# Performance work log

Measured on AMD Instinct MI355X. Metric: run time of the kernel, lower is better.

## Reference

```python
import jax, jax.numpy as jnp
import numpy as np

K = 16  # kNN neighbors (KnnEncoder default)


def _bn(h, g, s):
    # eval-mode BatchNorm with running mean 0 / var 1 folded into affine
    return h * g + s


def setup_inputs() -> dict:
    key = jax.random.key(0)
    cnt = [0]
    def nk():
        cnt[0] += 1
        return jax.random.fold_in(key, cnt[0])
    B, N = 4, 4096
    def W(i, o):
        return jax.random.normal(nk(), (i, o), jnp.float32) / np.float32(i) ** 0.5
    def bias(d):
        return jnp.zeros((d,), jnp.float32)
    def gamma(d):
        return jnp.ones((d,), jnp.float32) + 0.1 * jax.random.normal(nk(), (d,), jnp.float32)
    def beta(d):
        return 0.1 * jax.random.normal(nk(), (d,), jnp.float32)
    inp = dict(
        pos=jax.random.normal(nk(), (B, N, 3), jnp.float32),
        query_point_idx=jax.random.randint(nk(), (B,), 0, N),
        # PointNetConv local MLP: 6 -> 64 -> 128 -> 256 (plain last)
        cw1=W(6, 64), cb1=bias(64), cg1=gamma(64), cs1=beta(64),
        cw2=W(64, 128), cb2=bias(128), cg2=gamma(128), cs2=beta(128),
        cw3=W(128, 256), cb3=bias(256),
        # GlobalSAModule MLP: 259 -> 256 -> 512 -> 1024 (plain last)
        sw1=W(259, 256), sb1=bias(256), sg1=gamma(256), ss1=beta(256),
        sw2=W(256, 512), sb2=bias(512), sg2=gamma(512), ss2=beta(512),
        sw3=W(512, 1024), sb3=bias(1024),
        # EdgeGraspPredictor: 1280 -> 512 -> 256 -> 16
        pw1=W(1280, 512), pb1=bias(512),
        pw2=W(512, 256), pb2=bias(256),
        pw3=W(256, 16), pb3=bias(16),
    )
    return inp


def reference(pos, query_point_idx, cw1, cb1, cg1, cs1, cw2, cb2, cg2, cs2, cw3, cb3,
              sw1, sb1, sg1, ss1, sw2, sb2, sg2, ss2, sw3, sb3,
              pw1, pb1, pw2, pb2, pw3, pb3):
    B, N, _ = pos.shape
    # kNN within each cloud (self included, as torch_geometric knn with x==y)
    d2 = jnp.sum((pos[:, :, None, :] - pos[:, None, :, :]) ** 2, axis=-1)  # [B,N,N]
    _, idx = jax.lax.top_k(-d2, K)  # [B,N,K] targets for each source point n
    nbr = jax.vmap(lambda p, i: p[i])(pos, idx)  # [B,N,K,3] target positions
    # PointNetConv message: cat([x_j = pos_src, pos_src - pos_tgt])
    src = jnp.broadcast_to(pos[:, :, None, :], (B, N, K, 3))
    h = jnp.concatenate([src, src - nbr], axis=-1)  # [B,N,K,6]
    h = jnp.maximum(_bn(h @ cw1 + cb1, cg1, cs1), 0.0)
    h = jnp.maximum(_bn(h @ cw2 + cb2, cg2, cs2), 0.0)
    m = h @ cw3 + cb3  # [B,N,K,256] per-edge messages
    # scatter-max aggregation at target nodes (every node has its self edge)
    tgt = (idx + (jnp.arange(B) * N)[:, None, None]).reshape(-1)
    x = jax.ops.segment_max(m.reshape(-1, m.shape[-1]), tgt, num_segments=B * N)
    x = x.reshape(B, N, -1)  # [B,N,256] per-point features
    # GlobalSAModule: pointwise MLP then global max pool per cloud
    g = jnp.concatenate([x, pos], axis=-1)  # [B,N,259]
    g = jnp.maximum(_bn(g @ sw1 + sb1, sg1, ss1), 0.0)
    g = jnp.maximum(_bn(g @ sw2 + sb2, sg2, ss2), 0.0)
    g = g @ sw3 + sb3  # [B,N,1024]
    scene = jnp.max(g, axis=1)  # [B,1024]
    # gather query point feature, concat with scene feature, predictor MLP
    q = query_point_idx + jnp.arange(B) * N
    point_feat = x.reshape(B * N, -1)[q]  # [B,256]
    ef = jnp.concatenate([point_feat, scene], axis=-1)  # [B,1280]
    h = jnp.maximum(ef @ pw1 + pb1, 0.0)
    h = jnp.maximum(h @ pw2 + pb2, 0.0)
    return h @ pw3 + pb3  # [B,16]
```

## Files before the change

kernel.cpp:

```cpp
#include <hip/hip_runtime.h>

#define BB 4
#define NN 4096
#define KK 16

typedef unsigned short u16;
typedef unsigned int   u32;
typedef unsigned long long u64;

typedef __attribute__((ext_vector_type(8))) short bf16x8;
typedef __attribute__((ext_vector_type(4))) float f32x4;

__device__ __forceinline__ float b2f(u16 x){ return __uint_as_float(((u32)x) << 16); }
__device__ __forceinline__ u16 f2b(float f){
    u32 u = __float_as_uint(f);
    u32 r = (u + 0x7FFFu + ((u >> 16) & 1u)) >> 16;
    return (u16)r;
}
__device__ __forceinline__ u32 fmap(float f){
    u32 u = __float_as_uint(f);
    return (u & 0x80000000u) ? ~u : (u | 0x80000000u);
}
__device__ __forceinline__ float funmap(u32 u){
    u32 v = (u & 0x80000000u) ? (u ^ 0x80000000u) : ~u;
    return __uint_as_float(v);
}

#define N_ARR 27
__device__ const int ASZ[N_ARR] = {
    49152, 384, 64, 64, 64, 8192, 128, 128, 128, 32768, 256,
    66304, 256, 256, 256, 131072, 512, 512, 512, 524288, 1024,
    655360, 512, 131072, 256, 4096, 16 };
__device__ const int AOFF[N_ARR] = {
    0, 49152, 49536, 49600, 49664, 49728, 57920, 58048, 58176, 58304, 91072,
    91328, 157632, 157888, 158144, 158400, 289472, 289984, 290496, 291008, 815296,
    816320, 1471680, 1472192, 1603264, 1603520, 1607616 };

struct Ptrs { const void* p[N_ARR]; };

#define O_POS 0
#define O_CW1 49152
#define O_CB1 49536
#define O_CG1 49600
#define O_CS1 49664
#define O_CB2 57920
#define O_CG2 58048
#define O_CS2 58176
#define O_CB3 91072
#define O_SW1 91328
#define O_SB1 157632
#define O_SG1 157888
#define O_SS1 158144
#define O_SB2 289472
#define O_SG2 289984
#define O_SS2 290496
#define O_SB3 815296
#define O_PW1 816320
#define O_PB1 1471680
#define O_PW2 1472192
#define O_PB2 1603264
#define O_PW3 1603520
#define O_PB3 1607616

__global__ void detect_kernel(const u16* __restrict__ pos_u16, u32* __restrict__ flag){
    __shared__ int cnt;
    if (threadIdx.x == 0) cnt = 0;
    __syncthreads();
    int c = 0;
    #pragma unroll
    for (int s = 0; s < 4; ++s){
        u16 u = pos_u16[2*(threadIdx.x*4 + s)];
        int e = (u >> 7) & 0xFF;
        c += (e >= 0x68 && e <= 0x82) ? 1 : 0;
    }
    atomicAdd(&cnt, c);
    __syncthreads();
    if (threadIdx.x == 0) *flag = (cnt >= 512) ? 1u : 0u;
}

__device__ __forceinline__ void pack_one_src(const void* __restrict__ src, bool isbf,
                                             u16* __restrict__ dst, int tot, int log2n,
                                             int g, int T){
    const int nmask = (1 << log2n) - 1;
    for (int id = g; id < tot; id += T){
        int i = id & 7, lg = (id >> 3) & 3;
        int rest = id >> 5;
        int n = rest & nmask;
        int ks = rest >> log2n;
        int si = (ks*32 + lg*8 + i) << log2n | n;
        dst[id] = isbf ? ((const u16*)src)[si] : f2b(((const float*)src)[si]);
    }
}

__global__ __launch_bounds__(256) void prep_kernel(Ptrs pt, const u32* __restrict__ flagp,
        float* __restrict__ dst, float* __restrict__ psoa,
        u16* __restrict__ wp2, u16* __restrict__ wp3,
        u16* __restrict__ swp1, u16* __restrict__ swp2, u16* __restrict__ swp3){
    const bool isbf = (*flagp != 0);
    const int T = gridDim.x * 256;
    const int g = blockIdx.x * 256 + threadIdx.x;
    #pragma unroll
    for (int a = 0; a < N_ARR; ++a){
        if (a == 5 || a == 9 || a == 15 || a == 19) continue;
        const int sz = ASZ[a], off = AOFF[a];
        if (isbf){
            const u16* s = (const u16*)pt.p[a];
            for (int i = g; i < sz; i += T) dst[off + i] = b2f(s[i]);
        } else {
            const float* s = (const float*)pt.p[a];
            for (int i = g; i < sz; i += T) dst[off + i] = s[i];
        }
    }
    for (int i = g; i < BB*NN; i += T){
        float x, y, z;
        if (isbf){
            const u16* s = (const u16*)pt.p[0];
            x = b2f(s[3*i]); y = b2f(s[3*i+1]); z = b2f(s[3*i+2]);
        } else {
            const float* s = (const float*)pt.p[0];
            x = s[3*i]; y = s[3*i+1]; z = s[3*i+2];
        }
        psoa[i] = x; psoa[BB*NN + i] = y; psoa[2*BB*NN + i] = z;
    }
    pack_one_src(pt.p[5],  isbf, wp2,    8192,  7, g, T);
    pack_one_src(pt.p[9],  isbf, wp3,   32768,  8, g, T);
    pack_one_src(pt.p[11], isbf, swp1,  65536,  8, g, T);
    pack_one_src(pt.p[15], isbf, swp2, 131072,  9, g, T);
    pack_one_src(pt.p[19], isbf, swp3, 524288, 10, g, T);
}

#define QCAP 192
__device__ __forceinline__ void refine16(u64* __restrict__ buf, int& cnt, float& tau, int lane){
    u64 loc[3];
    #pragma unroll
    for (int q = 0; q < 3; ++q){
        int p = lane + (q << 6);
        loc[q] = (p < cnt) ? buf[p] : ~0ull;
    }
    u64 m = ~0ull;
    #pragma unroll
    for (int r = 0; r < KK; ++r){
        m = loc[0];
        m = loc[1] < m ? loc[1] : m;
        m = loc[2] < m ? loc[2] : m;
        #pragma unroll
        for (int off = 32; off > 0; off >>= 1){
            u64 o = __shfl_xor(m, off);
            m = o < m ? o : m;
        }
        if (lane == r) buf[r] = m;
        #pragma unroll
        for (int q = 0; q < 3; ++q) if (loc[q] == m) loc[q] = ~0ull;
    }
    cnt = KK;
    tau = __uint_as_float((u32)(m >> 32));
}

__global__ __launch_bounds__(512) void knn_kernel(const float* __restrict__ psoa,
                                                  int* __restrict__ knn_out,
                                                  u32* __restrict__ deg){
    __shared__ __align__(16) u64 kbuf[16*QCAP];
    const int b  = blockIdx.x >> 8;
    const int i0 = (blockIdx.x & 255) << 4;
    const float* px = psoa + b*NN;
    const float* py = psoa + BB*NN + b*NN;
    const float* pz = psoa + 2*BB*NN + b*NN;
    const int tid = threadIdx.x;
    const int lane = tid & 63;
    const int wv = tid >> 6;
    const int iA = i0 + wv*2, iB = iA + 1;
    const float ax = px[iA], ay = py[iA], az = pz[iA];
    const float bx = px[iB], by = py[iB], bz = pz[iB];
    u64* bufA = kbuf + (wv*2)*QCAP;
    u64* bufB = bufA + QCAP;

    float tauA = 3.0e38f, tauB = 3.0e38f;
    int cntA = 0, cntB = 0;
    for (int t = 0; t < 64; t += 8){
        float cx[8], cy[8], cz[8];
        #pragma unroll
        for (int c = 0; c < 8; ++c){
            int j = lane + ((t + c) << 6);
            cx[c] = px[j]; cy[c] = py[j]; cz[c] = pz[j];
        }
        #pragma unroll
        for (int c = 0; c < 8; ++c){
            int j = lane + ((t + c) << 6);
            float dxA = ax - cx[c], dyA = ay - cy[c], dzA = az - cz[c];
            float d2A = __fadd_rn(__fadd_rn(__fmul_rn(dxA,dxA), __fmul_rn(dyA,dyA)), __fmul_rn(dzA,dzA));
            float dxB = bx - cx[c], dyB = by - cy[c], dzB = bz - cz[c];
            float d2B = __fadd_rn(__fadd_rn(__fmul_rn(dxB,dxB), __fmul_rn(dyB,dyB)), __fmul_rn(dzB,dzB));
            bool pA = (d2A <= tauA);
            u64 balA = __ballot(pA);
            if (balA){
                int nins = __popcll(balA);
                if (cntA + nins > QCAP) refine16(bufA, cntA, tauA, lane);
                if (pA){
                    int ofs = __popcll(balA & ((1ull << lane) - 1ull));
                    bufA[cntA + ofs] = (((u64)__float_as_uint(d2A)) << 32) | (u32)j;
                }
                cntA += nins;
            }
            bool pB = (d2B <= tauB);
            u64 balB = __ballot(pB);
            if (balB){
                int nins = __popcll(balB);
                if (cntB + nins > QCAP) refine16(bufB, cntB, tauB, lane);
                if (pB){
                    int ofs = __popcll(balB & ((1ull << lane) - 1ull));
                    bufB[cntB + ofs] = (((u64)__float_as_uint(d2B)) << 32) | (u32)j;
                }
                cntB += nins;
            }
        }
    }
    refine16(bufA, cntA, tauA, lane);
    refine16(bufB, cntB, tauB, lane);
    if (lane < KK){
        u64 kA = bufA[lane];
        int jA = (int)(u32)(kA & 0xFFFFFFFFu);
        knn_out[((size_t)(b*NN + iA))*KK + lane] = jA;
        atomicAdd(deg + (b << 12) + jA, 1u);
        u64 kB = bufB[lane];
        int jB = (int)(u32)(kB & 0xFFFFFFFFu);
        knn_out[((size_t)(b*NN + iB))*KK + lane] = jB;
        atomicAdd(deg + (b << 12) + jB, 1u);
    }
}

__global__ __launch_bounds__(1024) void scan_kernel(const u32* __restrict__ deg,
                                                    int* __restrict__ rowstart, u32* __restrict__ cursor){
    __shared__ int lsum[1024];
    const int tid = threadIdx.x;
    const int base = tid * 16;
    int loc[16]; int s = 0;
    #pragma unroll
    for (int q = 0; q < 16; ++q){ loc[q] = (int)deg[base+q]; s += loc[q]; }
    lsum[tid] = s;
    __syncthreads();
    int acc = s;
    for (int ofs = 1; ofs < 1024; ofs <<= 1){
        int t = (tid >= ofs) ? lsum[tid-ofs] : 0;
        __syncthreads();
        acc += t; lsum[tid] = acc;
        __syncthreads();
    }
    int excl = acc - s;
    #pragma unroll
    for (int q = 0; q < 16; ++q){
        rowstart[base+q] = excl; cursor[base+q] = (u32)excl; excl += loc[q];
    }
    if (tid == 1023) rowstart[16384] = excl;
}

__global__ __launch_bounds__(256) void fill_kernel(const int* __restrict__ knn,
                                                   u32* __restrict__ cursor, int* __restrict__ csr){
    int e = blockIdx.x*256 + threadIdx.x;
    int b = e >> 16;
    int t = (b << 12) + knn[e];
    u32 pos = atomicAdd(cursor + t, 1u);
    csr[pos] = e;
}

__device__ __forceinline__ bf16x8 ldfrag(const u16* h, int row, int kofs, int rowstride){
    u32 byte = (u32)((row*rowstride + kofs)*2) ^ (u32)((row & 7) << 4);
    return *(const bf16x8*)((const char*)h + byte);
}
__device__ __forceinline__ void st16(u16* h, int row, int col, int rowstride, float v){
    u32 byte = (u32)((row*rowstride + col)*2) ^ (u32)((row & 7) << 4);
    *(u16*)((char*)h + byte) = f2b(v);
}

__global__ __launch_bounds__(256, 2) void edge_kernel(
    const float* __restrict__ conv, const int* __restrict__ knn,
    const int* __restrict__ rowstart, const int* __restrict__ csr,
    const u16* __restrict__ wp2, const u16* __restrict__ wp3,
    u16* __restrict__ xh)
{
    __shared__ float in6[6][64];
    __shared__ int   lts[64];
    __shared__ int   rs_l[17];
    __shared__ float scw1[384];
    __shared__ float sc1[64], sh1[64];
    __shared__ __align__(16) u16 h1s[64*64];
    __shared__ __align__(16) u16 h2s[64*128];
    __shared__ u32 lsx[16*256];

    const float* posf = conv + O_POS;
    const float* cb1 = conv + O_CB1; const float* cg1 = conv + O_CG1; const float* cs1 = conv + O_CS1;

    const int tid = threadIdx.x;
    const int w   = tid >> 6;
    const int l   = tid & 63;
    const int t0  = blockIdx.x << 4;
    const int b   = t0 >> 12;

    if (tid < 64){ float g1 = cg1[tid]; sc1[tid]=g1; sh1[tid]=cb1[tid]*g1 + cs1[tid]; }
    if (tid < 17) rs_l[tid] = rowstart[t0 + tid];
    for (int u = tid; u < 384; u += 256) scw1[u] = conv[O_CW1 + u];
    #pragma unroll
    for (int q = 0; q < 16; ++q) lsx[q*256 + tid] = 0u;

    const int lr = l & 15, lg = l >> 4;
    const int colb2 = w << 5;
    const int colb3 = w << 6;

    float sc2v[2], sh2v[2], bs3v[4];
    #pragma unroll
    for (int nt = 0; nt < 2; ++nt){
        int c = colb2 + nt*16 + lr;
        float g2 = conv[O_CG2 + c];
        sc2v[nt] = g2; sh2v[nt] = conv[O_CB2 + c]*g2 + conv[O_CS2 + c];
    }
    #pragma unroll
    for (int nt = 0; nt < 4; ++nt) bs3v[nt] = conv[O_CB3 + colb3 + nt*16 + lr];

    __syncthreads();
    const int segstart = rs_l[0], segend = rs_l[16];
    const int nchunk = (segend - segstart + 63) >> 6;

    int curl = -1;
    float run[4];
    #pragma unroll
    for (int nt = 0; nt < 4; ++nt) run[nt] = 0.f;

    for (int ch = 0; ch < nchunk; ++ch){
        __syncthreads();
        if (tid < 64){
            int gpos = segstart + (ch << 6) + tid;
            int lt = -1;
            float ax=0,ay=0,az=0,dx=0,dy=0,dz=0;
            if (gpos < segend){
                lt = 0;
                #pragma unroll
                for (int q = 1; q < 16; ++q) lt += (gpos >= rs_l[q]) ? 1 : 0;
                int e = csr[gpos];
                int i = (e >> 4) & (NN - 1);
                int j = knn[e];
                const float* pi = posf + ((size_t)(b*NN + i))*3;
                const float* pj = posf + ((size_t)(b*NN + j))*3;
                ax = pi[0]; ay = pi[1]; az = pi[2];
                dx = ax - pj[0]; dy = ay - pj[1]; dz = az - pj[2];
            }
            lts[tid] = lt;
            in6[0][tid]=ax; in6[1][tid]=ay; in6[2][tid]=az;
            in6[3][tid]=dx; in6[4][tid]=dy; in6[5][tid]=dz;
        }
        __syncthreads();

        {
            const int e = tid & 63, c0g = (tid >> 6) << 4;
            float a0=in6[0][e], a1=in6[1][e], a2=in6[2][e],
                  a3=in6[3][e], a4=in6[4][e], a5=in6[5][e];
            u32 pk[8];
            #pragma unroll
            for (int ci = 0; ci < 16; ++ci){
                int cc = c0g + ci;
                float acc = a0*scw1[cc]     + a1*scw1[64+cc]  + a2*scw1[128+cc]
                          + a3*scw1[192+cc] + a4*scw1[256+cc] + a5*scw1[320+cc];
                float v = fmaxf(acc*sc1[cc] + sh1[cc], 0.f);
                u32 h = (u32)f2b(v);
                if (ci & 1) pk[ci >> 1] |= h << 16; else pk[ci >> 1] = h;
            }
            u32 base = (u32)(e*128 + c0g*2);
            u32 swz  = (u32)((e & 7) << 4);
            *(uint4*)((char*)h1s + (base ^ swz))        = make_uint4(pk[0],pk[1],pk[2],pk[3]);
            *(uint4*)((char*)h1s + ((base + 16) ^ swz)) = make_uint4(pk[4],pk[5],pk[6],pk[7]);
        }
        __syncthreads();

        {
            f32x4 acc2[4][2];
            #pragma unroll
            for (int mt = 0; mt < 4; ++mt)
                #pragma unroll
                for (int nt = 0; nt < 2; ++nt) acc2[mt][nt] = (f32x4){0.f,0.f,0.f,0.f};
            #pragma unroll
            for (int ks = 0; ks < 2; ++ks){
                bf16x8 bf[2];
                #pragma unroll
                for (int nt = 0; nt < 2; ++nt)
                    bf[nt] = *(const bf16x8*)(wp2 + (((ks*128 + colb2 + nt*16 + lr) << 2) + lg)*8);
                #pragma unroll
                for (int mt = 0; mt < 4; ++mt){
                    bf16x8 a = ldfrag(h1s, mt*16 + lr, ks*32 + lg*8, 64);
                    #pragma unroll
                    for (int nt = 0; nt < 2; ++nt)
                        acc2[mt][nt] = __builtin_amdgcn_mfma_f32_16x16x32_bf16(a, bf[nt], acc2[mt][nt], 0, 0, 0);
                }
            }
            #pragma unroll
            for (int mt = 0; mt < 4; ++mt)
                #pragma unroll
                for (int nt = 0; nt < 2; ++nt)
                    #pragma unroll
                    for (int r = 0; r < 4; ++r){
                        int row = mt*16 + lg*4 + r;
                        float v = fmaxf(acc2[mt][nt][r]*sc2v[nt] + sh2v[nt], 0.f);
                        st16(h2s, row, colb2 + nt*16 + lr, 128, v);
                    }
        }
        __syncthreads();

        {
            f32x4 acc3[4][4];
            #pragma unroll
            for (int mt = 0; mt < 4; ++mt)
                #pragma unroll
                for (int nt = 0; nt < 4; ++nt) acc3[mt][nt] = (f32x4){0.f,0.f,0.f,0.f};
            #pragma unroll
            for (int ks = 0; ks < 4; ++ks){
                bf16x8 bf[4];
                #pragma unroll
                for (int nt = 0; nt < 4; ++nt)
                    bf[nt] = *(const bf16x8*)(wp3 + (((ks*256 + colb3 + nt*16 + lr) << 2) + lg)*8);
                #pragma unroll
                for (int mt = 0; mt < 4; ++mt){
                    bf16x8 a = ldfrag(h2s, mt*16 + lr, ks*32 + lg*8, 128);
                    #pragma unroll
                    for (int nt = 0; nt < 4; ++nt)
                        acc3[mt][nt] = __builtin_amdgcn_mfma_f32_16x16x32_bf16(a, bf[nt], acc3[mt][nt], 0, 0, 0);
                }
            }
            #pragma unroll
            for (int mt = 0; mt < 4; ++mt)
                #pragma unroll
                for (int r = 0; r < 4; ++r){
                    int row = mt*16 + lg*4 + r;
                    int lt = lts[row];
                    if (lt != curl){
                        if (curl >= 0){
                            #pragma unroll
                            for (int nt = 0; nt < 4; ++nt)
                                atomicMax(&lsx[curl*256 + colb3 + nt*16 + lr], fmap(run[nt]));
                        }
                        curl = lt;
                        #pragma unroll
                        for (int nt = 0; nt < 4; ++nt) run[nt] = acc3[mt][nt][r] + bs3v[nt];
                    } else {
                        #pragma unroll
                        for (int nt = 0; nt < 4; ++nt) run[nt] = fmaxf(run[nt], acc3[mt][nt][r] + bs3v[nt]);
                    }
                }
        }
    }
    if (curl >= 0){
        #pragma unroll
        for (int nt = 0; nt < 4; ++nt)
            atomicMax(&lsx[curl*256 + colb3 + nt*16 + lr], fmap(run[nt]));
    }
    __syncthreads();
    #pragma unroll
    for (int q = 0; q < 16; ++q)
        xh[((size_t)(t0+q))*256 + tid] = f2b(funmap(lsx[q*256 + tid]));
}

__global__ __launch_bounds__(256, 3) void sa_kernel(
    const float* __restrict__ conv, const u16* __restrict__ xh,
    const u16* __restrict__ swp1, const u16* __restrict__ swp2, const u16* __restrict__ swp3,
    u32* __restrict__ scene_map)
{
    __shared__ __align__(16) u16 h1s[32*256];
    __shared__ __align__(16) u16 h2s[32*512];
    __shared__ float spw[3][256];
    __shared__ float spx[32], spy[32], spz[32];

    const int tid = threadIdx.x;
    const int w   = tid >> 6;
    const int l   = tid & 63;
    const int lr  = l & 15, lg = l >> 4;
    const int b   = blockIdx.x >> 7;
    const int n0  = (blockIdx.x & 127) << 5;
    const u16* xrow = xh + ((size_t)(b*NN + n0))*256;

    if (tid < 96){
        int p = tid & 31, d = tid >> 5;
        float v = conv[O_POS + ((size_t)(b*NN + n0 + p))*3 + d];
        if (d == 0) spx[p] = v; else if (d == 1) spy[p] = v; else spz[p] = v;
    }
    for (int u = tid; u < 768; u += 256)
        spw[u >> 8][u & 255] = conv[O_SW1 + (256 + (u >> 8))*256 + (u & 255)];
    __syncthreads();

    {
        const int c0 = w << 6;
        float sc1v[4], sh1v[4];
        #pragma unroll
        for (int nt = 0; nt < 4; ++nt){
            int cc = c0 + nt*16 + lr;
            float g = conv[O_SG1 + cc];
            sc1v[nt] = g; sh1v[nt] = conv[O_SB1 + cc]*g + conv[O_SS1 + cc];
        }
        f32x4 acc[2][4];
        #pragma unroll
        for (int mt = 0; mt < 2; ++mt)
            #pragma unroll
            for (int nt = 0; nt < 4; ++nt)
                #pragma unroll
                for (int r = 0; r < 4; ++r){
                    int row = mt*16 + lg*4 + r;
                    int cc  = c0 + nt*16 + lr;
                    acc[mt][nt][r] = spx[row]*spw[0][cc] + spy[row]*spw[1][cc] + spz[row]*spw[2][cc];
                }
        #pragma unroll
        for (int ks = 0; ks < 8; ++ks){
            bf16x8 bf[4];
            #pragma unroll
            for (int nt = 0; nt < 4; ++nt)
                bf[nt] = *(const bf16x8*)(swp1 + (((ks*256 + c0 + nt*16 + lr) << 2) + lg)*8);
            #pragma unroll
            for (int mt = 0; mt < 2; ++mt){
                bf16x8 a = *(const bf16x8*)(xrow + (mt*16 + lr)*256 + ks*32 + lg*8);
                #pragma unroll
                for (int nt = 0; nt < 4; ++nt)
                    acc[mt][nt] = __builtin_amdgcn_mfma_f32_16x16x32_bf16(a, bf[nt], acc[mt][nt], 0, 0, 0);
            }
        }
        #pragma unroll
        for (int mt = 0; mt < 2; ++mt)
            #pragma unroll
            for (int nt = 0; nt < 4; ++nt)
                #pragma unroll
                for (int r = 0; r < 4; ++r){
                    int row = mt*16 + lg*4 + r;
                    float v = fmaxf(acc[mt][nt][r]*sc1v[nt] + sh1v[nt], 0.f);
                    st16(h1s, row, c0 + nt*16 + lr, 256, v);
                }
    }
    __syncthreads();

    {
        const int c0 = w << 7;
        float sc2v[8], sh2v[8];
        #pragma unroll
        for (int nt = 0; nt < 8; ++nt){
            int cc = c0 + nt*16 + lr;
            float g = conv[O_SG2 + cc];
            sc2v[nt] = g; sh2v[nt] = conv[O_SB2 + cc]*g + conv[O_SS2 + cc];
        }
        f32x4 acc[2][8];
        #pragma unroll
        for (int mt = 0; mt < 2; ++mt)
            #pragma unroll
            for (int nt = 0; nt < 8; ++nt) acc[mt][nt] = (f32x4){0.f,0.f,0.f,0.f};
        #pragma unroll
        for (int ks = 0; ks < 8; ++ks){
            bf16x8 bf[8];
            #pragma unroll
            for (int nt = 0; nt < 8; ++nt)
                bf[nt] = *(const bf16x8*)(swp2 + (((ks*512 + c0 + nt*16 + lr) << 2) + lg)*8);
            #pragma unroll
            for (int mt = 0; mt < 2; ++mt){
                bf16x8 a = ldfrag(h1s, mt*16 + lr, ks*32 + lg*8, 256);
                #pragma unroll
                for (int nt = 0; nt < 8; ++nt)
                    acc[mt][nt] = __builtin_amdgcn_mfma_f32_16x16x32_bf16(a, bf[nt], acc[mt][nt], 0, 0, 0);
            }
        }
        #pragma unroll
        for (int mt = 0; mt < 2; ++mt)
            #pragma unroll
            for (int nt = 0; nt < 8; ++nt)
                #pragma unroll
                for (int r = 0; r < 4; ++r){
                    int row = mt*16 + lg*4 + r;
                    float v = fmaxf(acc[mt][nt][r]*sc2v[nt] + sh2v[nt], 0.f);
                    st16(h2s, row, c0 + nt*16 + lr, 512, v);
                }
    }
    __syncthreads();

    #pragma unroll
    for (int half = 0; half < 2; ++half){
        const int c0 = (half << 9) + (w << 7);
        f32x4 acc[2][8];
        #pragma unroll
        for (int mt = 0; mt < 2; ++mt)
            #pragma unroll
            for (int nt = 0; nt < 8; ++nt) acc[mt][nt] = (f32x4){0.f,0.f,0.f,0.f};
        #pragma unroll
        for (int ks = 0; ks < 16; ++ks){
            bf16x8 bf[8];
            #pragma unroll
            for (int nt = 0; nt < 8; ++nt)
                bf[nt] = *(const bf16x8*)(swp3 + (((ks*1024 + c0 + nt*16 + lr) << 2) + lg)*8);
            #pragma unroll
            for (int mt = 0; mt < 2; ++mt){
                bf16x8 a = ldfrag(h2s, mt*16 + lr, ks*32 + lg*8, 512);
                #pragma unroll
                for (int nt = 0; nt < 8; ++nt)
                    acc[mt][nt] = __builtin_amdgcn_mfma_f32_16x16x32_bf16(a, bf[nt], acc[mt][nt], 0, 0, 0);
            }
        }
        #pragma unroll
        for (int nt = 0; nt < 8; ++nt){
            float v = acc[0][nt][0];
            #pragma unroll
            for (int mt = 0; mt < 2; ++mt)
                #pragma unroll
                for (int r = 0; r < 4; ++r) v = fmaxf(v, acc[mt][nt][r]);
            v = fmaxf(v, __shfl_xor(v, 16));
            v = fmaxf(v, __shfl_xor(v, 32));
            if (lg == 0){
                int cc = c0 + nt*16 + lr;
                atomicMax(scene_map + (b << 10) + cc, fmap(v + conv[O_SB3 + cc]));
            }
        }
    }
}

__global__ __launch_bounds__(128) void head1_kernel(
    const float* __restrict__ conv,
    const u16* __restrict__ xh, const u32* __restrict__ scene_map, const int* __restrict__ qidx,
    float* __restrict__ h1out)
{
    __shared__ float ef[1280];
    __shared__ float psum[4][32];
    const float* pw1 = conv + O_PW1; const float* pb1 = conv + O_PB1;
    const int b  = blockIdx.x >> 4;
    const int c0 = (blockIdx.x & 15) << 5;
    const int tid = threadIdx.x;
    const int q = qidx[b];
    for (int u = tid; u < 1280; u += 128){
        float v;
        if (u < 256) v = b2f(xh[(((size_t)(b*NN + q)) << 8) + u]);
        else         v = funmap(scene_map[(b << 10) + (u - 256)]);
        ef[u] = v;
    }
    __syncthreads();
    const int c = c0 + (tid & 31);
    const int rc = tid >> 5;
    float acc = 0.f;
    for (int r = rc*320; r < rc*320 + 320; ++r) acc += ef[r] * pw1[r*512 + c];
    psum[rc][tid & 31] = acc;
    __syncthreads();
    if (tid < 32){
        float a = psum[0][tid] + psum[1][tid] + psum[2][tid] + psum[3][tid] + pb1[c0 + tid];
        h1out[(b << 9) + c0 + tid] = fmaxf(a, 0.f);
    }
}

__global__ __launch_bounds__(256) void head2_kernel(
    const float* __restrict__ conv, const float* __restrict__ h1in,
    const u32* __restrict__ flagp, void* __restrict__ outv)
{
    __shared__ float h1[4][512];
    __shared__ float h2[4][256];
    const float* pw2 = conv + O_PW2; const float* pb2 = conv + O_PB2;
    const float* pw3 = conv + O_PW3; const float* pb3 = conv + O_PB3;
    const int tid = threadIdx.x;
    for (int u = tid; u < 2048; u += 256) h1[u >> 9][u & 511] = h1in[u];
    __syncthreads();
    for (int o = tid; o < 1024; o += 256){
        int b = o >> 8, c = o & 255;
        float acc = pb2[c];
        for (int r = 0; r < 512; ++r) acc += h1[b][r] * pw2[r*256 + c];
        h2[b][c] = fmaxf(acc, 0.f);
    }
    __syncthreads();
    if (tid < 64){
        int b = tid >> 4, c = tid & 15;
        float acc = pb3[c];
        for (int r = 0; r < 256; ++r) acc += h2[b][r] * pw3[r*16 + c];
        if (*flagp) ((u16*)outv)[tid] = f2b(acc);
        else        ((float*)outv)[tid] = acc;
    }
}

extern "C" void kernel_launch(void* const* d_in, const int* in_sizes, int n_in,
                              void* d_out, int out_size, void* d_ws, size_t ws_size,
                              hipStream_t stream){
    (void)in_sizes; (void)n_in; (void)out_size; (void)ws_size;
    const int* qidx = (const int*)d_in[1];

    char* ws = (char*)d_ws;
    u32*  flag      = (u32*)ws;
    float* conv     = (float*)(ws + 1024);
    u16*  wp2       = (u16*)(ws + 6432768);
    u16*  wp3       = (u16*)(ws + 6449152);
    u16*  swp1      = (u16*)(ws + 6514688);
    u16*  swp2      = (u16*)(ws + 6645760);
    u16*  swp3      = (u16*)(ws + 6907904);
    int*  knn       = (int*)(ws + 7956480);
    u32*  deg       = (u32*)(ws + 9005056);
    u32*  scene_map = (u32*)(ws + 9070592);
    int*  rowstart  = (int*)(ws + 9086976);
    u32*  cursor    = (u32*)(ws + 9152576);
    int*  csr       = (int*)(ws + 9218112);
    u16*  xh        = (u16*)(ws + 10266688);
    float* h1ws     = (float*)(ws + 18655296);
    float* psoa     = (float*)(ws + 18663488);

    Ptrs pt;
    pt.p[0] = d_in[0];
    for (int k = 1; k < N_ARR; ++k) pt.p[k] = d_in[k + 1];

    hipMemsetAsync(ws + 9005056, 0, 81920, stream);

    detect_kernel <<<1, 256, 0, stream>>>((const u16*)d_in[0], flag);
    prep_kernel   <<<512, 256, 0, stream>>>(pt, flag, conv, psoa, wp2, wp3, swp1, swp2, swp3);
    knn_kernel <<<1024, 512, 0, stream>>>(psoa, knn, deg);
    scan_kernel<<<1, 1024, 0, stream>>>(deg, rowstart, cursor);
    fill_kernel<<<1024, 256, 0, stream>>>(knn, cursor, csr);
    edge_kernel<<<1024, 256, 0, stream>>>(conv, knn, rowstart, csr, wp2, wp3, xh);
    sa_kernel  <<<512, 256, 0, stream>>>(conv, xh, swp1, swp2, swp3, scene_map);
    head1_kernel<<<64, 128, 0, stream>>>(conv, xh, scene_map, qidx, h1ws);
    head2_kernel<<<1, 256, 0, stream>>>(conv, h1ws, flag, (void*)d_out);
}
```

Baseline: 371.0 us.

## Sort points by x and prune kNN search with a sweep-window bound

Adds a per-cloud bitonic sort of points by x coordinate, then has the kNN kernel scan candidates outward from each query's sorted position. The scan stops once the x-gap on both sides exceeds the current 16th-nearest distance. This replaces the brute-force scan of all 4096 candidates per query with a pruned scan. It adds a sort kernel running on only 4 blocks, and the pruning can be weak for 3D Gaussian data sorted on one axis. Tie ordering among equal distances may differ because indices are remapped through the sort.

```diff
diff --git a/kernel.cpp b/kernel.cpp
--- a/kernel.cpp
+++ b/kernel.cpp
@@ -129,6 +129,40 @@
     pack_one_src(pt.p[19], isbf, swp3, 524288, 10, g, T);
 }
 
+__global__ __launch_bounds__(1024) void sort_kernel(const float* __restrict__ psoa,
+        float* __restrict__ xs, float* __restrict__ ys, float* __restrict__ zs,
+        int* __restrict__ sidx){
+    __shared__ u64 s[NN];
+    const int b = blockIdx.x;
+    const int tid = threadIdx.x;
+    const float* px = psoa + b*NN;
+    const float* py = psoa + BB*NN + b*NN;
+    const float* pz = psoa + 2*BB*NN + b*NN;
+    for (int i = tid; i < NN; i += 1024)
+        s[i] = (((u64)fmap(px[i])) << 32) | (u32)i;
+    __syncthreads();
+    for (int ksz = 2; ksz <= NN; ksz <<= 1){
+        for (int jj = ksz >> 1; jj > 0; jj >>= 1){
+            for (int t = tid; t < NN/2; t += 1024){
+                int i  = ((t & ~(jj-1)) << 1) | (t & (jj-1));
+                int ix = i | jj;
+                u64 a = s[i], v = s[ix];
+                bool up = ((i & ksz) == 0);
+                if ((a > v) == up){ s[i] = v; s[ix] = a; }
+            }
+            __syncthreads();
+        }
+    }
+    for (int r = tid; r < NN; r += 1024){
+        u64 kv = s[r];
+        int oi = (int)(u32)(kv & 0xFFFFFFFFu);
+        xs[b*NN + r] = funmap((u32)(kv >> 32));
+        ys[b*NN + r] = py[oi];
+        zs[b*NN + r] = pz[oi];
+        sidx[b*NN + r] = oi;
+    }
+}
+
 #define QCAP 192
 __device__ __forceinline__ void refine16(u64* __restrict__ buf, int& cnt, float& tau, int lane){
     u64 loc[3];
@@ -156,74 +190,80 @@
     tau = __uint_as_float((u32)(m >> 32));
 }
 
-__global__ __launch_bounds__(512) void knn_kernel(const float* __restrict__ psoa,
-                                                  int* __restrict__ knn_out,
-                                                  u32* __restrict__ deg){
+__global__ __launch_bounds__(512) void knn_kernel(
+        const float* __restrict__ xs, const float* __restrict__ ys,
+        const float* __restrict__ zs, const int* __restrict__ sidx,
+        int* __restrict__ knn_out, u32* __restrict__ deg){
     __shared__ __align__(16) u64 kbuf[16*QCAP];
     const int b  = blockIdx.x >> 8;
-    const int i0 = (blockIdx.x & 255) << 4;
-    const float* px = psoa + b*NN;
-    const float* py = psoa + BB*NN + b*NN;
-    const float* pz = psoa + 2*BB*NN + b*NN;
+    const int r0 = (blockIdx.x & 255) << 4;
+    const float* X = xs + b*NN;
+    const float* Y = ys + b*NN;
+    const float* Z = zs + b*NN;
+    const int*   S = sidx + b*NN;
     const int tid = threadIdx.x;
     const int lane = tid & 63;
     const int wv = tid >> 6;
-    const int iA = i0 + wv*2, iB = iA + 1;
-    const float ax = px[iA], ay = py[iA], az = pz[iA];
-    const float bx = px[iB], by = py[iB], bz = pz[iB];
+    const int rA = r0 + wv*2, rB = rA + 1;
+    const float axq = X[rA], ayq = Y[rA], azq = Z[rA];
+    const float bxq = X[rB], byq = Y[rB], bzq = Z[rB];
     u64* bufA = kbuf + (wv*2)*QCAP;
     u64* bufB = bufA + QCAP;
 
     float tauA = 3.0e38f, tauB = 3.0e38f;
     int cntA = 0, cntB = 0;
-    for (int t = 0; t < 64; t += 8){
-        float cx[8], cy[8], cz[8];
-        #pragma unroll
-        for (int c = 0; c < 8; ++c){
-            int j = lane + ((t + c) << 6);
-            cx[c] = px[j]; cy[c] = py[j]; cz[c] = pz[j];
-        }
-        #pragma unroll
-        for (int c = 0; c < 8; ++c){
-            int j = lane + ((t + c) << 6);
-            float dxA = ax - cx[c], dyA = ay - cy[c], dzA = az - cz[c];
-            float d2A = __fadd_rn(__fadd_rn(__fmul_rn(dxA,dxA), __fmul_rn(dyA,dyA)), __fmul_rn(dzA,dzA));
-            float dxB = bx - cx[c], dyB = by - cy[c], dzB = bz - cz[c];
-            float d2B = __fadd_rn(__fadd_rn(__fmul_rn(dxB,dxB), __fmul_rn(dyB,dyB)), __fmul_rn(dzB,dzB));
-            bool pA = (d2A <= tauA);
-            u64 balA = __ballot(pA);
-            if (balA){
-                int nins = __popcll(balA);
-                if (cntA + nins > QCAP) refine16(bufA, cntA, tauA, lane);
-                if (pA){
-                    int ofs = __popcll(balA & ((1ull << lane) - 1ull));
-                    bufA[cntA + ofs] = (((u64)__float_as_uint(d2A)) << 32) | (u32)j;
-                }
-                cntA += nins;
-            }
-            bool pB = (d2B <= tauB);
-            u64 balB = __ballot(pB);
-            if (balB){
-                int nins = __popcll(balB);
-                if (cntB + nins > QCAP) refine16(bufB, cntB, tauB, lane);
-                if (pB){
-                    int ofs = __popcll(balB & ((1ull << lane) - 1ull));
-                    bufB[cntB + ofs] = (((u64)__float_as_uint(d2B)) << 32) | (u32)j;
-                }
-                cntB += nins;
-            }
-        }
+    for (int k = 0; k < 128; ++k){
+        int j = (lane < 32) ? (rA - 1 - (k << 5) - lane)
+                            : (rA + (k << 5) + (lane - 32));
+        bool inr = ((u32)j < (u32)NN);
+        int ja = inr ? j : rA;
+        float cx = X[ja], cy = Y[ja], cz = Z[ja];
+        int sorig = S[ja];
+        float dxA = axq - cx, dyA = ayq - cy, dzA = azq - cz;
+        float d2A = __fadd_rn(__fadd_rn(__fmul_rn(dxA,dxA), __fmul_rn(dyA,dyA)), __fmul_rn(dzA,dzA));
+        float dxB = bxq - cx, dyB = byq - cy, dzB = bzq - cz;
+        float d2B = __fadd_rn(__fadd_rn(__fmul_rn(dxB,dxB), __fmul_rn(dyB,dyB)), __fmul_rn(dzB,dzB));
+        bool pA = inr && (d2A <= tauA);
+        u64 balA = __ballot(pA);
+        if (balA){
+            int nins = __popcll(balA);
+            if (cntA + nins > QCAP) refine16(bufA, cntA, tauA, lane);
+            if (pA){
+                int ofs = __popcll(balA & ((1ull << lane) - 1ull));
+                bufA[cntA + ofs] = (((u64)__float_as_uint(d2A)) << 32) | (u32)sorig;
+            }
+            cntA += nins;
+        }
+        bool pB = inr && (d2B <= tauB);
+        u64 balB = __ballot(pB);
+        if (balB){
+            int nins = __popcll(balB);
+            if (cntB + nins > QCAP) refine16(bufB, cntB, tauB, lane);
+            if (pB){
+                int ofs = __popcll(balB & ((1ull << lane) - 1ull));
+                bufB[cntB + ofs] = (((u64)__float_as_uint(d2B)) << 32) | (u32)sorig;
+            }
+            cntB += nins;
+        }
+        int lo = rA - ((k + 1) << 5) - 1;
+        int hi = rA + ((k + 1) << 5);
+        float xlo = (lo >= 0) ? X[lo] : -3.0e38f;
+        float xhi = (hi < NN) ? X[hi] :  3.0e38f;
+        float dLa = axq - xlo, dRa = xhi - axq;
+        float dLb = bxq - xlo, dRb = xhi - bxq;
+        if (dLa*dLa > tauA && dRa*dRa > tauA && dLb*dLb > tauB && dRb*dRb > tauB) break;
     }
     refine16(bufA, cntA, tauA, lane);
     refine16(bufB, cntB, tauB, lane);
+    const int origA = S[rA], origB = S[rB];
     if (lane < KK){
         u64 kA = bufA[lane];
         int jA = (int)(u32)(kA & 0xFFFFFFFFu);
-        knn_out[((size_t)(b*NN + iA))*KK + lane] = jA;
+        knn_out[((size_t)(b*NN + origA))*KK + lane] = jA;
         atomicAdd(deg + (b << 12) + jA, 1u);
         u64 kB = bufB[lane];
         int jB = (int)(u32)(kB & 0xFFFFFFFFu);
-        knn_out[((size_t)(b*NN + iB))*KK + lane] = jB;
+        knn_out[((size_t)(b*NN + origB))*KK + lane] = jB;
         atomicAdd(deg + (b << 12) + jB, 1u);
     }
 }
@@ -690,6 +730,10 @@
     u16*  xh        = (u16*)(ws + 10266688);
     float* h1ws     = (float*)(ws + 18655296);
     float* psoa     = (float*)(ws + 18663488);
+    float* xs       = (float*)(ws + 18860096);
+    float* ys       = (float*)(ws + 18925632);
+    float* zs       = (float*)(ws + 18991168);
+    int*   sidx     = (int*)(ws + 19056704);
 
     Ptrs pt;
     pt.p[0] = d_in[0];
@@ -699,7 +743,8 @@
 
     detect_kernel <<<1, 256, 0, stream>>>((const u16*)d_in[0], flag);
     prep_kernel   <<<512, 256, 0, stream>>>(pt, flag, conv, psoa, wp2, wp3, swp1, swp2, swp3);
-    knn_kernel <<<1024, 512, 0, stream>>>(psoa, knn, deg);
+    sort_kernel   <<<BB, 1024, 0, stream>>>(psoa, xs, ys, zs, sidx);
+    knn_kernel <<<1024, 512, 0, stream>>>(xs, ys, zs, sidx, knn, deg);
     scan_kernel<<<1, 1024, 0, stream>>>(deg, rowstart, cursor);
     fill_kernel<<<1024, 256, 0, stream>>>(knn, cursor, csr);
     edge_kernel<<<1024, 256, 0, stream>>>(conv, knn, rowstart, csr, wp2, wp3, xh);
```

Measured after the change: 394.2 us. +6.2%, slower.
